# Performance work log

Measured on AMD Instinct MI355X. Metric: run time of the kernel, lower is better.

Reference implementation:

```python
import jax, jax.numpy as jnp
import numpy as np

NUM_TOKENS = 8192
D_MODEL = 512
D_FF = 1024
NUM_EXPERTS = 8
TOP_K = 2


def setup_inputs() -> dict:
    key = jax.random.key(0)
    k_x, k_r, k_w1, k_w2 = jax.random.split(key, 4)
    x = jax.random.normal(k_x, (NUM_TOKENS, D_MODEL), dtype=jnp.float32)
    # Router weight [num_experts, d_model]
    w_router = jax.random.normal(k_r, (NUM_EXPERTS, D_MODEL), dtype=jnp.float32) * 0.02
    # Expert weights stored as [E, N, K] (kernel convention: y = x @ W.T)
    w1 = jax.random.normal(k_w1, (NUM_EXPERTS, D_FF, D_MODEL), dtype=jnp.float32) * 0.02
    w2 = jax.random.normal(k_w2, (NUM_EXPERTS, D_MODEL, D_FF), dtype=jnp.float32) * 0.02
    return {"x": x, "w_router": w_router, "w1": w1, "w2": w2}


def reference(x, w_router, w1, w2):
    # Router: softmax over experts, top-k selection, renormalized gates
    logits = jnp.einsum("td,ed->te", x, w_router)            # [T, E]
    probs = jax.nn.softmax(logits, axis=-1)
    top_vals, top_idx = jax.lax.top_k(probs, TOP_K)           # [T, k]
    top_vals = top_vals / jnp.sum(top_vals, axis=-1, keepdims=True)

    # Combine weights per (token, expert): topk weight if selected else 0.
    # out[t] = sum_e gate[t,e] * W2[e] @ silu(W1[e] @ x[t])
    out = jnp.zeros_like(x)
    for e in range(NUM_EXPERTS):
        gate_e = jnp.sum(jnp.where(top_idx == e, top_vals, 0.0), axis=-1)  # [T]
        h = jax.nn.silu(jnp.einsum("td,fd->tf", x, w1[e]))                 # [T, d_ff]
        y = jnp.einsum("tf,df->td", h, w2[e])                              # [T, d]
        out = out + gate_e[:, None] * y
    return out
```

## Files before the change

### kernel.cpp

```cpp
#include <hip/hip_runtime.h>
#include <hip/hip_bf16.h>

#define NT 8192
#define DM 512
#define DF 1024
#define NE 8
#define MAXROWS (NT*2)

typedef __bf16 bf16_8 __attribute__((ext_vector_type(8)));
typedef float  f32_4  __attribute__((ext_vector_type(4)));
typedef unsigned short us8 __attribute__((ext_vector_type(8)));

__device__ inline unsigned short f2bf(float f) {
    unsigned int u = __float_as_uint(f);
    u = u + 0x7fffu + ((u >> 16) & 1u);
    return (unsigned short)(u >> 16);
}

__device__ inline bf16_8 as_bf(us8 v) { return __builtin_bit_cast(bf16_8, v); }

__global__ __launch_bounds__(256) void cast_kernel(const float* __restrict__ in,
                                                   unsigned short* __restrict__ out,
                                                   int n4) {
    int i = blockIdx.x * 256 + threadIdx.x;
    if (i >= n4) return;
    float4 v = ((const float4*)in)[i];
    ushort4 o;
    o.x = f2bf(v.x); o.y = f2bf(v.y); o.z = f2bf(v.z); o.w = f2bf(v.w);
    ((ushort4*)out)[i] = o;
}

__global__ __launch_bounds__(256) void router_kernel(const float* __restrict__ x,
                                                     const float* __restrict__ wr,
                                                     int* __restrict__ eidx,
                                                     float2* __restrict__ gates) {
    const int wid = threadIdx.x >> 6;
    const int lane = threadIdx.x & 63;
    const int t = blockIdx.x * 4 + wid;

    const float4* xrow = (const float4*)(x + (size_t)t * DM);
    float4 xv0 = xrow[lane * 2];
    float4 xv1 = xrow[lane * 2 + 1];

    float logit[NE];
#pragma unroll
    for (int e = 0; e < NE; ++e) {
        const float4* wrow = (const float4*)(wr + (size_t)e * DM);
        float4 w0 = wrow[lane * 2];
        float4 w1v = wrow[lane * 2 + 1];
        float s = xv0.x * w0.x + xv0.y * w0.y + xv0.z * w0.z + xv0.w * w0.w
                + xv1.x * w1v.x + xv1.y * w1v.y + xv1.z * w1v.z + xv1.w * w1v.w;
#pragma unroll
        for (int off = 32; off >= 1; off >>= 1) s += __shfl_xor(s, off);
        logit[e] = s;
    }

    if (lane == 0) {
        int i0 = 0; float m0 = logit[0];
#pragma unroll
        for (int e = 1; e < NE; ++e) if (logit[e] > m0) { m0 = logit[e]; i0 = e; }
        int i1 = -1; float m1 = -1e30f;
#pragma unroll
        for (int e = 0; e < NE; ++e) if (e != i0 && logit[e] > m1) { m1 = logit[e]; i1 = e; }
        float d = expf(m1 - m0);
        float g0 = 1.0f / (1.0f + d);
        float g1 = 1.0f - g0;
        eidx[t] = i0 | (i1 << 8);
        gates[t] = make_float2(g0, g1);
    }
}

__global__ __launch_bounds__(256) void build_lists_kernel(const int* __restrict__ eidx,
                                                          const float2* __restrict__ gates,
                                                          int* __restrict__ counts,
                                                          int* __restrict__ token_list,
                                                          float* __restrict__ gate_list) {
    const int e = blockIdx.x;
    const int tid = threadIdx.x;
    const int wid = tid >> 6, lane = tid & 63;
    __shared__ int wsum[4];
    __shared__ int base;
    if (tid == 0) base = 0;
    __syncthreads();
    for (int c = 0; c < NT; c += 256) {
        int t = c + tid;
        int ei = eidx[t];
        int i0 = ei & 0xff, i1 = (ei >> 8) & 0xff;
        bool match0 = (i0 == e), match1 = (i1 == e);
        bool m = match0 || match1;
        unsigned long long mask = __ballot(m);
        if (lane == 0) wsum[wid] = __popcll(mask);
        __syncthreads();
        int pre = 0;
#pragma unroll
        for (int w = 0; w < 4; ++w) if (w < wid) pre += wsum[w];
        int tot = wsum[0] + wsum[1] + wsum[2] + wsum[3];
        if (m) {
            int pos = base + pre + __popcll(mask & ((1ULL << lane) - 1ULL));
            token_list[e * NT + pos] = t;
            float2 g = gates[t];
            gate_list[e * NT + pos] = match0 ? g.x : g.y;
        }
        __syncthreads();
        if (tid == 0) base += tot;
        __syncthreads();
    }
    if (tid == 0) counts[e] = base;
}

__global__ void scan_kernel(const int* __restrict__ counts, int* __restrict__ offsets) {
    if (threadIdx.x == 0) {
        int s = 0;
        for (int e = 0; e < NE; ++e) { offsets[e] = s; s += counts[e]; }
    }
}

template <bool G1>
__global__ __launch_bounds__(256) void moe_gemm(const unsigned short* __restrict__ Abase,
                                                const unsigned short* __restrict__ Wbase,
                                                unsigned short* __restrict__ h_out,
                                                float* __restrict__ out,
                                                const int* __restrict__ counts,
                                                const int* __restrict__ offsets,
                                                const int* __restrict__ token_list,
                                                const float* __restrict__ gate_list) {
    constexpr int K = G1 ? DM : DF;
    constexpr int NCOLS = G1 ? DF : DM;
    const int e = blockIdx.z;
    const int cnt = counts[e];
    const int row0 = blockIdx.y * 64;
    if (row0 >= cnt) return;
    const int col0 = blockIdx.x * 64;

    __shared__ __align__(16) unsigned short Alds[64][40];
    __shared__ __align__(16) unsigned short Blds[64][40];

    const int tr = threadIdx.x >> 2;
    const int tc = threadIdx.x & 3;

    int rloc = min(row0 + tr, cnt - 1);
    const unsigned short* Arow;
    if (G1) {
        int tok = token_list[e * NT + rloc];
        Arow = Abase + (size_t)tok * K;
    } else {
        Arow = Abase + (size_t)(offsets[e] + rloc) * K;
    }
    const unsigned short* Brow = Wbase + ((size_t)e * NCOLS + (col0 + tr)) * K;

    const int wid = threadIdx.x >> 6;
    const int lane = threadIdx.x & 63;
    const int wr = wid >> 1, wc = wid & 1;
    const int lrow = lane & 15;
    const int kc = lane >> 4;

    f32_4 acc[2][2];
#pragma unroll
    for (int m = 0; m < 2; ++m)
#pragma unroll
        for (int n = 0; n < 2; ++n) acc[m][n] = (f32_4){0.f, 0.f, 0.f, 0.f};

    for (int k0 = 0; k0 < K; k0 += 32) {
        us8 av = *(const us8*)(Arow + k0 + tc * 8);
        us8 bv = *(const us8*)(Brow + k0 + tc * 8);
        __syncthreads();
        *(us8*)&Alds[tr][tc * 8] = av;
        *(us8*)&Blds[tr][tc * 8] = bv;
        __syncthreads();

        bf16_8 a[2], b[2];
#pragma unroll
        for (int m = 0; m < 2; ++m)
            a[m] = as_bf(*(const us8*)&Alds[wr * 32 + m * 16 + lrow][kc * 8]);
#pragma unroll
        for (int n = 0; n < 2; ++n)
            b[n] = as_bf(*(const us8*)&Blds[wc * 32 + n * 16 + lrow][kc * 8]);
#pragma unroll
        for (int m = 0; m < 2; ++m)
#pragma unroll
            for (int n = 0; n < 2; ++n)
                acc[m][n] = __builtin_amdgcn_mfma_f32_16x16x32_bf16(a[m], b[n], acc[m][n], 0, 0, 0);
    }

#pragma unroll
    for (int m = 0; m < 2; ++m) {
#pragma unroll
        for (int n = 0; n < 2; ++n) {
#pragma unroll
            for (int q = 0; q < 4; ++q) {
                int lr = wr * 32 + m * 16 + (lane >> 4) * 4 + q;
                int lc = wc * 32 + n * 16 + (lane & 15);
                int r = row0 + lr;
                if (r < cnt) {
                    float v = acc[m][n][q];
                    if (G1) {
                        v = v / (1.0f + expf(-v));
                        h_out[(size_t)(offsets[e] + r) * DF + col0 + lc] = f2bf(v);
                    } else {
                        float g = gate_list[e * NT + r];
                        int tok = token_list[e * NT + r];
                        atomicAdd(&out[(size_t)tok * DM + col0 + lc], g * v);
                    }
                }
            }
        }
    }
}

extern "C" void kernel_launch(void* const* d_in, const int* in_sizes, int n_in,
                              void* d_out, int out_size, void* d_ws, size_t ws_size,
                              hipStream_t stream) {
    const float* x   = (const float*)d_in[0];
    const float* wrt = (const float*)d_in[1];
    const float* w1  = (const float*)d_in[2];
    const float* w2  = (const float*)d_in[3];
    float* out = (float*)d_out;

    char* ws = (char*)d_ws;
    size_t o = 0;
    auto alloc = [&](size_t bytes) { size_t r = o; o += (bytes + 255) & ~255UL; return r; };
    unsigned short* x_bf  = (unsigned short*)(ws + alloc((size_t)NT * DM * 2));
    unsigned short* w1_bf = (unsigned short*)(ws + alloc((size_t)NE * DF * DM * 2));
    unsigned short* w2_bf = (unsigned short*)(ws + alloc((size_t)NE * DM * DF * 2));
    unsigned short* h_bf  = (unsigned short*)(ws + alloc((size_t)MAXROWS * DF * 2));
    int*   counts     = (int*)(ws + alloc(NE * 4));
    int*   offsets    = (int*)(ws + alloc(NE * 4));
    int*   token_list = (int*)(ws + alloc((size_t)NE * NT * 4));
    float* gate_list  = (float*)(ws + alloc((size_t)NE * NT * 4));
    int*   eidx       = (int*)(ws + alloc((size_t)NT * 4));
    float2* gates     = (float2*)(ws + alloc((size_t)NT * 8));

    hipMemsetAsync(out, 0, (size_t)NT * DM * 4, stream);

    int n4x = NT * DM / 4;
    cast_kernel<<<(n4x + 255) / 256, 256, 0, stream>>>(x, x_bf, n4x);
    int n4w = NE * DF * DM / 4;
    cast_kernel<<<(n4w + 255) / 256, 256, 0, stream>>>(w1, w1_bf, n4w);
    cast_kernel<<<(n4w + 255) / 256, 256, 0, stream>>>(w2, w2_bf, n4w);

    router_kernel<<<NT / 4, 256, 0, stream>>>(x, wrt, eidx, gates);
    build_lists_kernel<<<NE, 256, 0, stream>>>(eidx, gates, counts, token_list, gate_list);
    scan_kernel<<<1, 64, 0, stream>>>(counts, offsets);

    moe_gemm<true><<<dim3(DF / 64, NT / 64, NE), 256, 0, stream>>>(
        x_bf, w1_bf, h_bf, nullptr, counts, offsets, token_list, gate_list);
    moe_gemm<false><<<dim3(DM / 64, NT / 64, NE), 256, 0, stream>>>(
        h_bf, w2_bf, nullptr, out, counts, offsets, token_list, gate_list);
}
```

Before: 174.4 us.

## Enlarge MoE GEMM tiles to 128x128 with direct global-to-LDS loads and swizzle

```diff
diff --git a/kernel.cpp b/kernel.cpp
--- a/kernel.cpp
+++ b/kernel.cpp
@@ -18,6 +18,12 @@
 }
 
 __device__ inline bf16_8 as_bf(us8 v) { return __builtin_bit_cast(bf16_8, v); }
+
+__device__ inline void gld16(const unsigned short* g, unsigned short* l) {
+    __builtin_amdgcn_global_load_lds(
+        (const __attribute__((address_space(1))) unsigned int*)g,
+        (__attribute__((address_space(3))) unsigned int*)l, 16, 0, 0);
+}
 
 __global__ __launch_bounds__(256) void cast_kernel(const float* __restrict__ in,
                                                    unsigned short* __restrict__ out,
@@ -128,74 +134,98 @@
     constexpr int NCOLS = G1 ? DF : DM;
     const int e = blockIdx.z;
     const int cnt = counts[e];
-    const int row0 = blockIdx.y * 64;
+    const int row0 = blockIdx.y * 128;
     if (row0 >= cnt) return;
-    const int col0 = blockIdx.x * 64;
-
-    __shared__ __align__(16) unsigned short Alds[64][40];
-    __shared__ __align__(16) unsigned short Blds[64][40];
-
-    const int tr = threadIdx.x >> 2;
-    const int tc = threadIdx.x & 3;
-
-    int rloc = min(row0 + tr, cnt - 1);
-    const unsigned short* Arow;
-    if (G1) {
-        int tok = token_list[e * NT + rloc];
-        Arow = Abase + (size_t)tok * K;
-    } else {
-        Arow = Abase + (size_t)(offsets[e] + rloc) * K;
-    }
-    const unsigned short* Brow = Wbase + ((size_t)e * NCOLS + (col0 + tr)) * K;
-
-    const int wid = threadIdx.x >> 6;
-    const int lane = threadIdx.x & 63;
+    const int col0 = blockIdx.x * 128;
+    const int off_e = offsets[e];
+
+    __shared__ __align__(16) unsigned short Alds[128 * 32];
+    __shared__ __align__(16) unsigned short Blds[128 * 32];
+
+    const int tid = threadIdx.x;
+    const int wid = tid >> 6;
+    const int lane = tid & 63;
+
+    const int c0 = wid * 128 + lane;
+    const int c1 = c0 + 64;
+    const int r0 = c0 >> 2, q0 = c0 & 3;
+    const int r1 = c1 >> 2, q1 = c1 & 3;
+    const int qs0 = q0 ^ (r0 & 3);
+    const int qs1 = q1 ^ (r1 & 3);
+
+    const unsigned short* gA0;
+    const unsigned short* gA1;
+    {
+        int rr0 = min(row0 + r0, cnt - 1);
+        int rr1 = min(row0 + r1, cnt - 1);
+        if (G1) {
+            gA0 = Abase + (size_t)token_list[e * NT + rr0] * K + qs0 * 8;
+            gA1 = Abase + (size_t)token_list[e * NT + rr1] * K + qs1 * 8;
+        } else {
+            gA0 = Abase + (size_t)(off_e + rr0) * K + qs0 * 8;
+            gA1 = Abase + (size_t)(off_e + rr1) * K + qs1 * 8;
+        }
+    }
+    const unsigned short* gB0 = Wbase + ((size_t)e * NCOLS + col0 + r0) * K + qs0 * 8;
+    const unsigned short* gB1 = Wbase + ((size_t)e * NCOLS + col0 + r1) * K + qs1 * 8;
+
+    unsigned short* ldsA0 = Alds + (wid * 128) * 8;
+    unsigned short* ldsA1 = Alds + (wid * 128 + 64) * 8;
+    unsigned short* ldsB0 = Blds + (wid * 128) * 8;
+    unsigned short* ldsB1 = Blds + (wid * 128 + 64) * 8;
+
     const int wr = wid >> 1, wc = wid & 1;
     const int lrow = lane & 15;
-    const int kc = lane >> 4;
-
-    f32_4 acc[2][2];
-#pragma unroll
-    for (int m = 0; m < 2; ++m)
-#pragma unroll
-        for (int n = 0; n < 2; ++n) acc[m][n] = (f32_4){0.f, 0.f, 0.f, 0.f};
+    const int kcs = (lane >> 4) ^ (lrow & 3);
+    const unsigned short* rdA[4];
+    const unsigned short* rdB[4];
+#pragma unroll
+    for (int m = 0; m < 4; ++m)
+        rdA[m] = Alds + (wr * 64 + m * 16 + lrow) * 32 + kcs * 8;
+#pragma unroll
+    for (int n = 0; n < 4; ++n)
+        rdB[n] = Blds + (wc * 64 + n * 16 + lrow) * 32 + kcs * 8;
+
+    f32_4 acc[4][4];
+#pragma unroll
+    for (int m = 0; m < 4; ++m)
+#pragma unroll
+        for (int n = 0; n < 4; ++n) acc[m][n] = (f32_4){0.f, 0.f, 0.f, 0.f};
 
     for (int k0 = 0; k0 < K; k0 += 32) {
-        us8 av = *(const us8*)(Arow + k0 + tc * 8);
-        us8 bv = *(const us8*)(Brow + k0 + tc * 8);
-        __syncthreads();
-        *(us8*)&Alds[tr][tc * 8] = av;
-        *(us8*)&Blds[tr][tc * 8] = bv;
-        __syncthreads();
-
-        bf16_8 a[2], b[2];
-#pragma unroll
-        for (int m = 0; m < 2; ++m)
-            a[m] = as_bf(*(const us8*)&Alds[wr * 32 + m * 16 + lrow][kc * 8]);
-#pragma unroll
-        for (int n = 0; n < 2; ++n)
-            b[n] = as_bf(*(const us8*)&Blds[wc * 32 + n * 16 + lrow][kc * 8]);
-#pragma unroll
-        for (int m = 0; m < 2; ++m)
-#pragma unroll
-            for (int n = 0; n < 2; ++n)
+        gld16(gA0 + k0, ldsA0);
+        gld16(gA1 + k0, ldsA1);
+        gld16(gB0 + k0, ldsB0);
+        gld16(gB1 + k0, ldsB1);
+        __syncthreads();
+
+        bf16_8 a[4], b[4];
+#pragma unroll
+        for (int m = 0; m < 4; ++m) a[m] = as_bf(*(const us8*)rdA[m]);
+#pragma unroll
+        for (int n = 0; n < 4; ++n) b[n] = as_bf(*(const us8*)rdB[n]);
+#pragma unroll
+        for (int m = 0; m < 4; ++m)
+#pragma unroll
+            for (int n = 0; n < 4; ++n)
                 acc[m][n] = __builtin_amdgcn_mfma_f32_16x16x32_bf16(a[m], b[n], acc[m][n], 0, 0, 0);
-    }
-
-#pragma unroll
-    for (int m = 0; m < 2; ++m) {
-#pragma unroll
-        for (int n = 0; n < 2; ++n) {
+        __syncthreads();
+    }
+
+#pragma unroll
+    for (int m = 0; m < 4; ++m) {
+#pragma unroll
+        for (int n = 0; n < 4; ++n) {
 #pragma unroll
             for (int q = 0; q < 4; ++q) {
-                int lr = wr * 32 + m * 16 + (lane >> 4) * 4 + q;
-                int lc = wc * 32 + n * 16 + (lane & 15);
+                int lr = wr * 64 + m * 16 + (lane >> 4) * 4 + q;
+                int lc = wc * 64 + n * 16 + (lane & 15);
                 int r = row0 + lr;
                 if (r < cnt) {
                     float v = acc[m][n][q];
                     if (G1) {
                         v = v / (1.0f + expf(-v));
-                        h_out[(size_t)(offsets[e] + r) * DF + col0 + lc] = f2bf(v);
+                        h_out[(size_t)(off_e + r) * DF + col0 + lc] = f2bf(v);
                     } else {
                         float g = gate_list[e * NT + r];
                         int tok = token_list[e * NT + r];
@@ -242,8 +272,8 @@
     build_lists_kernel<<<NE, 256, 0, stream>>>(eidx, gates, counts, token_list, gate_list);
     scan_kernel<<<1, 64, 0, stream>>>(counts, offsets);
 
-    moe_gemm<true><<<dim3(DF / 64, NT / 64, NE), 256, 0, stream>>>(
+    moe_gemm<true><<<dim3(DF / 128, NT / 128, NE), 256, 0, stream>>>(
         x_bf, w1_bf, h_bf, nullptr, counts, offsets, token_list, gate_list);
-    moe_gemm<false><<<dim3(DM / 64, NT / 64, NE), 256, 0, stream>>>(
+    moe_gemm<false><<<dim3(DM / 128, NT / 128, NE), 256, 0, stream>>>(
         h_bf, w2_bf, nullptr, out, counts, offsets, token_list, gate_list);
 }
```

New measurement: 164.5 us. 5.7% less time.
